# Optimization experiments

Measured on AMD Instinct MI355X. Metric: run time of the kernel, lower is better.

The kernel has to match this reference:

```python
import jax, jax.numpy as jnp
import numpy as np

B, S, D, H = 4, 1024, 512, 16
HD = D // H
SCALE = 1.0 / np.sqrt(HD).astype(np.float32)


def setup_inputs() -> dict:
    key = jax.random.key(0)
    ks = jax.random.split(key, 20)
    std = 1.0 / np.sqrt(D).astype(np.float32)
    def W(k):
        return jax.random.normal(k, (D, D), jnp.float32) * std
    def b(k):
        return jax.random.normal(k, (D,), jnp.float32) * 0.01
    return {
        "x": jax.random.normal(ks[0], (B, S, D), jnp.float32),
        "ln_g": jnp.ones((D,), jnp.float32),
        "ln_b": jnp.zeros((D,), jnp.float32),
        "Wfa": W(ks[1]), "bfa": b(ks[2]),
        "Whp": W(ks[3]), "bhp": b(ks[4]),
        "Wmg": W(ks[5]), "bmg": b(ks[6]),
        "Wq": W(ks[7]), "bq": b(ks[8]),
        "Wk": W(ks[9]), "bk": b(ks[10]),
        "Wv": W(ks[11]), "bv": b(ks[12]),
        "Wo": W(ks[13]), "bo": b(ks[14]),
    }


def reference(x, ln_g, ln_b, Wfa, bfa, Whp, bhp, Wmg, bmg, Wq, bq, Wk, bk, Wv, bv, Wo, bo):
    residual = x
    # LayerNorm
    mu = jnp.mean(x, axis=-1, keepdims=True)
    var = jnp.mean(jnp.square(x - mu), axis=-1, keepdims=True)
    xn = (x - mu) * jax.lax.rsqrt(var + 1e-5) * ln_g + ln_b

    def lin(h, W, bb):
        return h @ W + bb

    fa = lin(xn, Wfa, bfa).reshape(B, S, H, HD)            # flow anchors, per-head
    hf = lin(xn, Whp, bhp).reshape(B, S, H, HD)            # hierarchical features
    mg = jax.nn.sigmoid(lin(xn, Wmg, bmg)).reshape(B, S, H, HD)  # memory gates
    q = lin(xn, Wq, bq).reshape(B, S, H, HD)
    k = lin(xn, Wk, bk).reshape(B, S, H, HD)
    v = lin(xn, Wv, bv).reshape(B, S, H, HD)

    # anchor weights: softmax over the SEQUENCE axis (dim=1)
    anchor_w = jax.nn.softmax(fa, axis=1)                  # [B,S,H,HD]
    k_weighted = k * anchor_w

    scores = jnp.einsum("bshd,bthd->bsht", q, k_weighted) * SCALE  # [B,S,H,T]
    probs = jax.nn.softmax(scores, axis=2)                 # softmax over HEAD axis (non-standard)
    attn = jnp.einsum("bsht,bthd->bshd", probs, v)         # [B,S,H,HD]

    out = (attn * mg + hf).reshape(B, S, D)
    out = lin(out, Wo, bo)
    return out + residual
```

## Files before the change

### kernel.cpp

```cpp
#include <hip/hip_runtime.h>
#include <hip/hip_bf16.h>
#include <math.h>

#define BB 4
#define SS 1024
#define DD 512
#define HH 16
#define HD 32
#define NTOK (BB * SS)
#define NELEM ((size_t)NTOK * DD)
#define SCALE 0.17677669529663687f
#define SCLOG2E 0.25505526082484745f

typedef __attribute__((ext_vector_type(8))) __bf16 bf16x8;
typedef __attribute__((ext_vector_type(4))) __bf16 bf16x4;
typedef __attribute__((ext_vector_type(4))) float f32x4;
typedef __attribute__((ext_vector_type(4))) unsigned short us4;
typedef __attribute__((ext_vector_type(4))) short s16x4;

__device__ __forceinline__ void gload16(const void* g, void* l) {
    __builtin_amdgcn_global_load_lds(
        (const __attribute__((address_space(1))) void*)g,
        (__attribute__((address_space(3))) void*)l, 16, 0, 0);
}

__global__ __launch_bounds__(256) void ln_kernel(const float* __restrict__ x,
                                                 const float* __restrict__ g,
                                                 const float* __restrict__ bta,
                                                 __bf16* __restrict__ xn) {
    int row = blockIdx.x;
    int tid = threadIdx.x;
    const float* xr = x + (size_t)row * DD;
    float2 v = *reinterpret_cast<const float2*>(&xr[tid * 2]);
    float s1 = v.x + v.y;
    float s2 = v.x * v.x + v.y * v.y;
    for (int off = 32; off > 0; off >>= 1) {
        s1 += __shfl_down(s1, off);
        s2 += __shfl_down(s2, off);
    }
    __shared__ float r1[4], r2[4];
    int w = tid >> 6;
    if ((tid & 63) == 0) { r1[w] = s1; r2[w] = s2; }
    __syncthreads();
    s1 = r1[0] + r1[1] + r1[2] + r1[3];
    s2 = r2[0] + r2[1] + r2[2] + r2[3];
    float mu = s1 * (1.0f / DD);
    float var = s2 * (1.0f / DD) - mu * mu;
    float rstd = rsqrtf(var + 1e-5f);
    float2 gg = *reinterpret_cast<const float2*>(&g[tid * 2]);
    float2 bb = *reinterpret_cast<const float2*>(&bta[tid * 2]);
    __bf16* xp = xn + (size_t)row * DD + tid * 2;
    xp[0] = (__bf16)((v.x - mu) * rstd * gg.x + bb.x);
    xp[1] = (__bf16)((v.y - mu) * rstd * gg.y + bb.y);
}

struct W7 { const float* p[7]; };

__global__ __launch_bounds__(256) void wprep(W7 wp, __bf16* __restrict__ Wt) {
    int z = blockIdx.z;
    int kt = blockIdx.x, nt = blockIdx.y;
    const float* W = wp.p[z];
    __shared__ float lds[32][33];
    int tid = threadIdx.x;
    int r = tid >> 3, c4 = (tid & 7) * 4;
    float4 vv = *reinterpret_cast<const float4*>(W + (size_t)(kt * 32 + r) * DD + nt * 32 + c4);
    lds[r][c4 + 0] = vv.x; lds[r][c4 + 1] = vv.y;
    lds[r][c4 + 2] = vv.z; lds[r][c4 + 3] = vv.w;
    __syncthreads();
    __bf16* o = Wt + (size_t)z * DD * DD + (size_t)(nt * 32 + r) * DD + kt * 32 + c4;
    o[0] = (__bf16)lds[c4 + 0][r];
    o[1] = (__bf16)lds[c4 + 1][r];
    o[2] = (__bf16)lds[c4 + 2][r];
    o[3] = (__bf16)lds[c4 + 3][r];
}

struct GemmCfg { const float* bias[6]; void* out[6]; int mode[6]; };

__global__ __launch_bounds__(256) void mfma_gemm(const __bf16* __restrict__ A,
                                                 const __bf16* __restrict__ Wt0,
                                                 GemmCfg cfg,
                                                 const float* __restrict__ resid) {
    __shared__ __align__(16) char smem[49152];
    int z = blockIdx.z;
    const char* Ab8 = (const char*)A;
    const char* Bb8 = (const char*)(Wt0 + (size_t)z * DD * DD);
    int tid = threadIdx.x;
    int l = tid & 63, wid = tid >> 6;
    int lr = l & 15, lg = l >> 4;
    int wm = wid >> 1, wn = wid & 1;
    int bm = blockIdx.x * 128;
    int bn = blockIdx.y * 64;

    f32x4 acc[4][2];
#pragma unroll
    for (int i = 0; i < 4; ++i)
#pragma unroll
        for (int j = 0; j < 2; ++j) acc[i][j] = (f32x4){0.f, 0.f, 0.f, 0.f};

    auto stage = [&](int k0, int bsel) {
        char* base = smem + bsel * 24576;
#pragma unroll
        for (int i = 0; i < 4; ++i) {
            int r = wid * 32 + i * 8 + (l >> 3);
            int cb = ((l & 7) * 16) ^ ((r & 7) << 4);
            gload16(Ab8 + (size_t)(bm + r) * 1024 + k0 * 2 + cb,
                    base + wid * 4096 + i * 1024);
        }
#pragma unroll
        for (int i = 0; i < 2; ++i) {
            int r = wid * 16 + i * 8 + (l >> 3);
            int cb = ((l & 7) * 16) ^ ((r & 7) << 4);
            gload16(Bb8 + (size_t)(bn + r) * 1024 + k0 * 2 + cb,
                    base + 16384 + wid * 2048 + i * 1024);
        }
    };

    stage(0, 0);
    for (int ks = 0; ks < 8; ++ks) {
        __builtin_amdgcn_s_barrier();
        if (ks < 7) {
            stage((ks + 1) * 64, (ks + 1) & 1);
            asm volatile("s_waitcnt vmcnt(6)" ::: "memory");
        } else {
            asm volatile("s_waitcnt vmcnt(0)" ::: "memory");
        }
        __builtin_amdgcn_s_barrier();
        __builtin_amdgcn_sched_barrier(0);

        const char* cbase = smem + (ks & 1) * 24576;
#pragma unroll
        for (int kk = 0; kk < 2; ++kk) {
            bf16x8 af[4], wf[2];
#pragma unroll
            for (int mi = 0; mi < 4; ++mi) {
                int m = wm * 64 + mi * 16 + lr;
                af[mi] = *reinterpret_cast<const bf16x8*>(
                    cbase + m * 128 + ((kk * 64 + lg * 16) ^ ((m & 7) << 4)));
            }
#pragma unroll
            for (int ni = 0; ni < 2; ++ni) {
                int n = wn * 32 + ni * 16 + lr;
                wf[ni] = *reinterpret_cast<const bf16x8*>(
                    cbase + 16384 + n * 128 + ((kk * 64 + lg * 16) ^ ((n & 7) << 4)));
            }
            __builtin_amdgcn_s_setprio(1);
#pragma unroll
            for (int mi = 0; mi < 4; ++mi)
#pragma unroll
                for (int ni = 0; ni < 2; ++ni)
                    acc[mi][ni] = __builtin_amdgcn_mfma_f32_16x16x32_bf16(af[mi], wf[ni], acc[mi][ni], 0, 0, 0);
            __builtin_amdgcn_s_setprio(0);
        }
    }

    int bmw = bm + wm * 64;
    int bnw = bn + wn * 32;
    int mode = cfg.mode[z];
    const float* bias = cfg.bias[z];
    float bv[2] = {bias[bnw + lr], bias[bnw + 16 + lr]};
#pragma unroll
    for (int mi = 0; mi < 4; ++mi) {
#pragma unroll
        for (int ni = 0; ni < 2; ++ni) {
#pragma unroll
            for (int r = 0; r < 4; ++r) {
                int row = bmw + mi * 16 + lg * 4 + r;
                int col = bnw + ni * 16 + lr;
                float val = acc[mi][ni][r] + bv[ni];
                if (mode == 0) {
                    if (resid) val += resid[(size_t)row * DD + col];
                    ((float*)cfg.out[z])[(size_t)row * DD + col] = val;
                } else if (mode == 1) {
                    val = 1.0f / (1.0f + expf(-val));
                    ((__bf16*)cfg.out[z])[(size_t)row * DD + col] = (__bf16)val;
                } else if (mode == 3) {
                    ((__bf16*)cfg.out[z])[(size_t)row * DD + col] = (__bf16)(val * SCLOG2E);
                } else {
                    ((__bf16*)cfg.out[z])[(size_t)row * DD + col] = (__bf16)val;
                }
            }
        }
    }
}

__global__ __launch_bounds__(256) void anchor_partial(const __bf16* __restrict__ fa,
                                                      float* __restrict__ pmax,
                                                      float* __restrict__ psum) {
    int tx = threadIdx.x;
    int ty = threadIdx.y;
    int c = blockIdx.x * 64 + tx;
    int b = blockIdx.y;
    int sc = blockIdx.z;
    const __bf16* base = fa + ((size_t)(b * SS + sc * 256)) * DD + c;
    float m = -1e30f;
    for (int i = ty; i < 256; i += 4) m = fmaxf(m, (float)base[(size_t)i * DD]);
    __shared__ float red[4][64];
    red[ty][tx] = m;
    __syncthreads();
    float cm = fmaxf(fmaxf(red[0][tx], red[1][tx]), fmaxf(red[2][tx], red[3][tx]));
    float s = 0.f;
    for (int i = ty; i < 256; i += 4) s += expf((float)base[(size_t)i * DD] - cm);
    __syncthreads();
    red[ty][tx] = s;
    __syncthreads();
    if (ty == 0) {
        float tot = red[0][tx] + red[1][tx] + red[2][tx] + red[3][tx];
        int o = (b * 4 + sc) * DD + c;
        pmax[o] = cm;
        psum[o] = tot;
    }
}

__global__ __launch_bounds__(256) void anchor_merge(const float* __restrict__ pmax,
                                                    const float* __restrict__ psum,
                                                    float2* __restrict__ smscale) {
    int idx = blockIdx.x * 256 + threadIdx.x;
    int b = idx >> 9;
    int c = idx & 511;
    float M = -1e30f;
#pragma unroll
    for (int j = 0; j < 4; ++j) M = fmaxf(M, pmax[(b * 4 + j) * DD + c]);
    float Z = 0.f;
#pragma unroll
    for (int j = 0; j < 4; ++j) Z += psum[(b * 4 + j) * DD + c] * expf(pmax[(b * 4 + j) * DD + c] - M);
    smscale[idx] = make_float2(M, 1.0f / Z);
}

__global__ __launch_bounds__(256) void kweight(const __bf16* __restrict__ fa,
                                               const __bf16* __restrict__ kin,
                                               const float2* __restrict__ sm,
                                               __bf16* __restrict__ kw) {
    size_t f = ((size_t)blockIdx.x * 256 + threadIdx.x) * 8;
    int b = (int)(f >> 19);
    int c = (int)(f & 511);
    bf16x8 fv = *reinterpret_cast<const bf16x8*>(fa + f);
    bf16x8 kv = *reinterpret_cast<const bf16x8*>(kin + f);
    const float2* smb = sm + b * DD + c;
    bf16x8 o;
#pragma unroll
    for (int j = 0; j < 8; ++j) {
        float2 s = smb[j];
        o[j] = (__bf16)((float)kv[j] * expf((float)fv[j] - s.x) * s.y);
    }
    *reinterpret_cast<bf16x8*>(kw + f) = o;
}

__global__ __launch_bounds__(256) void vtrans(const __bf16* __restrict__ v,
                                              __bf16* __restrict__ vt) {
    int t0 = blockIdx.x * 32;
    int h = blockIdx.y;
    int b = blockIdx.z;
    __shared__ unsigned short lds[32][33];
    int tid = threadIdx.x;
    int r = tid >> 3, c4 = (tid & 7) * 4;
    const unsigned short* vp = (const unsigned short*)v + ((size_t)(b * SS + t0 + r)) * DD + h * 32 + c4;
    us4 val = *reinterpret_cast<const us4*>(vp);
    lds[r][c4 + 0] = val[0]; lds[r][c4 + 1] = val[1];
    lds[r][c4 + 2] = val[2]; lds[r][c4 + 3] = val[3];
    __syncthreads();
    us4 o;
    o[0] = lds[c4 + 0][r]; o[1] = lds[c4 + 1][r];
    o[2] = lds[c4 + 2][r]; o[3] = lds[c4 + 3][r];
    unsigned short* op = (unsigned short*)vt +
        ((size_t)(b * 128 + ((t0 + c4) >> 3)) * 512 + h * 32 + r) * 8 + (c4 & 7);
    *reinterpret_cast<us4*>(op) = o;
}

struct P4 { __bf16* p[4]; };

__global__ __launch_bounds__(512) void attn_mfma(const __bf16* __restrict__ q,
                                                 const __bf16* __restrict__ kw,
                                                 const __bf16* __restrict__ vt,
                                                 P4 ps) {
    __shared__ __align__(16) char smem[65536];
    int sgq = blockIdx.x;
    int b = blockIdx.y;
    int tp = blockIdx.z;
    int tid = threadIdx.x;
    int wid = tid >> 6;
    int lane = tid & 63;
    int lg = lane >> 4;
    int lr = lane & 15;
    int sgrp = wid & 1;
    int hq = wid >> 1;
    int hbase = hq * 4;
    int s0 = (sgq * 2 + sgrp) * 16;

    const __bf16* qbase = q + ((size_t)(b * SS + s0 + lr)) * DD + lg * 8;
    const char* kwb8 = (const char*)kw + (size_t)b * SS * DD * 2;
    const char* vtb8 = (const char*)vt + (size_t)b * 128 * 8192;

    bf16x8 qf[4];
#pragma unroll
    for (int hi = 0; hi < 4; ++hi)
        qf[hi] = *reinterpret_cast<const bf16x8*>(qbase + (hbase + hi) * 32);

    f32x4 acc[4][2];
#pragma unroll
    for (int hi = 0; hi < 4; ++hi) {
        acc[hi][0] = (f32x4){0.f, 0.f, 0.f, 0.f};
        acc[hi][1] = (f32x4){0.f, 0.f, 0.f, 0.f};
    }

    auto stage = [&](int tbase, int bsel) {
#pragma unroll
        for (int i = 0; i < 2; ++i) {
            int row = wid + i * 8;
            int colb = (lane * 16) ^ ((row & 15) << 4);
            gload16(kwb8 + (size_t)(tbase + row) * 1024 + colb,
                    smem + bsel * 16384 + row * 1024);
        }
#pragma unroll
        for (int i = 0; i < 2; ++i) {
            int blkid = wid + i * 8;
            gload16(vtb8 + (size_t)((tbase >> 3) + (blkid >> 3)) * 8192 + (blkid & 7) * 1024 + lane * 16,
                    smem + 32768 + bsel * 16384 + blkid * 1024);
        }
    };

    int tbase0 = tp * 256;
    stage(tbase0, 0);

    for (int tc = 0; tc < 256; tc += 16) {
        int cur = (tc >> 4) & 1;
        char* kwbuf = smem + cur * 16384;
        char* vtbuf = smem + 32768 + cur * 16384;
        char* xch = kwbuf + sgrp * 4096;

        asm volatile("s_waitcnt vmcnt(2)" ::: "memory");
        __builtin_amdgcn_s_barrier();
        __builtin_amdgcn_sched_barrier(0);

        f32x4 sc[4];
        bf16x8 ka[4];
#pragma unroll
        for (int hi = 0; hi < 4; ++hi)
            ka[hi] = *reinterpret_cast<const bf16x8*>(
                kwbuf + lr * 1024 + ((((hbase + hi) * 64) + lg * 16) ^ (lr << 4)));
        __builtin_amdgcn_s_setprio(1);
#pragma unroll
        for (int hi = 0; hi < 4; ++hi) {
            f32x4 z = (f32x4){0.f, 0.f, 0.f, 0.f};
            sc[hi] = __builtin_amdgcn_mfma_f32_16x16x32_bf16(ka[hi], qf[hi], z, 0, 0, 0);
        }
        __builtin_amdgcn_s_setprio(0);

        __builtin_amdgcn_s_barrier();
        __builtin_amdgcn_sched_barrier(0);

#pragma unroll
        for (int hi = 0; hi < 4; ++hi)
#pragma unroll
            for (int r = 0; r < 4; ++r) sc[hi][r] = exp2f(sc[hi][r]);
        f32x4 zsp = sc[0] + sc[1] + sc[2] + sc[3];
        *reinterpret_cast<f32x4*>(xch + hq * 1024 + lane * 16) = zsp;
        if (tc + 16 < 256) stage(tbase0 + tc + 16, cur ^ 1);
        asm volatile("s_waitcnt lgkmcnt(0)" ::: "memory");
        __builtin_amdgcn_s_barrier();
        __builtin_amdgcn_sched_barrier(0);

        f32x4 zt = zsp;
#pragma unroll
        for (int p = 0; p < 4; ++p)
            if (p != hq) zt += *reinterpret_cast<const f32x4*>(xch + p * 1024 + lane * 16);
        float inv[4];
#pragma unroll
        for (int r = 0; r < 4; ++r) inv[r] = __builtin_amdgcn_rcpf(zt[r]);
        bf16x4 pA[4];
#pragma unroll
        for (int hi = 0; hi < 4; ++hi)
#pragma unroll
            for (int r = 0; r < 4; ++r) pA[hi][r] = (__bf16)(sc[hi][r] * inv[r]);

        if (tc + 16 < 256) {
            asm volatile("s_waitcnt vmcnt(4)" ::: "memory");
        } else {
            asm volatile("s_waitcnt vmcnt(0)" ::: "memory");
        }
        __builtin_amdgcn_s_barrier();
        __builtin_amdgcn_sched_barrier(0);

        const char* vb = vtbuf + (lg >> 1) * 8192 + (lg & 1) * 8;
#pragma unroll
        for (int hi = 0; hi < 4; hi += 2) {
            s16x4 vf[4];
#pragma unroll
            for (int j = 0; j < 2; ++j) {
                int h = hbase + hi + j;
                vf[2 * j + 0] = *reinterpret_cast<const s16x4*>(vb + (h * 32 + lr) * 16);
                vf[2 * j + 1] = *reinterpret_cast<const s16x4*>(vb + (h * 32 + 16 + lr) * 16);
            }
            __builtin_amdgcn_s_setprio(1);
#pragma unroll
            for (int j = 0; j < 2; ++j) {
                s16x4 pa = __builtin_bit_cast(s16x4, pA[hi + j]);
                acc[hi + j][0] = __builtin_amdgcn_mfma_f32_16x16x16bf16_1k(pa, vf[2 * j + 0], acc[hi + j][0], 0, 0, 0);
                acc[hi + j][1] = __builtin_amdgcn_mfma_f32_16x16x16bf16_1k(pa, vf[2 * j + 1], acc[hi + j][1], 0, 0, 0);
            }
            __builtin_amdgcn_s_setprio(0);
        }
    }

    __bf16* pb = ps.p[tp] + ((size_t)(b * SS + s0)) * DD;
#pragma unroll
    for (int hi = 0; hi < 4; ++hi)
#pragma unroll
        for (int dh = 0; dh < 2; ++dh)
#pragma unroll
            for (int r = 0; r < 4; ++r)
                pb[(size_t)(lg * 4 + r) * DD + (hbase + hi) * 32 + dh * 16 + lr] = (__bf16)acc[hi][dh][r];
}

struct P4c { const __bf16* p[4]; };

__global__ __launch_bounds__(256) void combine_kernel(P4c ps,
                                                      const __bf16* __restrict__ mg,
                                                      const __bf16* __restrict__ hf,
                                                      __bf16* __restrict__ comb) {
    size_t f = ((size_t)blockIdx.x * 256 + threadIdx.x) * 8;
    float accv[8] = {0.f, 0.f, 0.f, 0.f, 0.f, 0.f, 0.f, 0.f};
#pragma unroll
    for (int i = 0; i < 4; ++i) {
        bf16x8 v = *reinterpret_cast<const bf16x8*>(ps.p[i] + f);
#pragma unroll
        for (int j = 0; j < 8; ++j) accv[j] += (float)v[j];
    }
    bf16x8 m = *reinterpret_cast<const bf16x8*>(mg + f);
    bf16x8 hh = *reinterpret_cast<const bf16x8*>(hf + f);
    bf16x8 o;
#pragma unroll
    for (int j = 0; j < 8; ++j) o[j] = (__bf16)(accv[j] * (float)m[j] + (float)hh[j]);
    *reinterpret_cast<bf16x8*>(comb + f) = o;
}

extern "C" void kernel_launch(void* const* d_in, const int* in_sizes, int n_in,
                              void* d_out, int out_size, void* d_ws, size_t ws_size,
                              hipStream_t stream) {
    const float* x    = (const float*)d_in[0];
    const float* ln_g = (const float*)d_in[1];
    const float* ln_b = (const float*)d_in[2];
    const float* Wfa  = (const float*)d_in[3];  const float* bfa = (const float*)d_in[4];
    const float* Whp  = (const float*)d_in[5];  const float* bhp = (const float*)d_in[6];
    const float* Wmg  = (const float*)d_in[7];  const float* bmg = (const float*)d_in[8];
    const float* Wq   = (const float*)d_in[9];  const float* bq  = (const float*)d_in[10];
    const float* Wk   = (const float*)d_in[11]; const float* bk  = (const float*)d_in[12];
    const float* Wv   = (const float*)d_in[13]; const float* bv  = (const float*)d_in[14];
    const float* Wo   = (const float*)d_in[15]; const float* bo  = (const float*)d_in[16];
    float* out = (float*)d_out;

    char* w8 = (char*)d_ws;
    __bf16* Wt   = (__bf16*)(w8 + ((size_t) 0 << 20));
    __bf16* xn   = (__bf16*)(w8 + ((size_t) 4 << 20));
    __bf16* fa   = (__bf16*)(w8 + ((size_t) 8 << 20));
    __bf16* hf   = (__bf16*)(w8 + ((size_t)12 << 20));
    __bf16* mg   = (__bf16*)(w8 + ((size_t)16 << 20));
    __bf16* q    = (__bf16*)(w8 + ((size_t)20 << 20));
    __bf16* k    = (__bf16*)(w8 + ((size_t)24 << 20));
    __bf16* v    = (__bf16*)(w8 + ((size_t)28 << 20));
    __bf16* kw   = (__bf16*)(w8 + ((size_t)32 << 20));
    __bf16* vt   = (__bf16*)(w8 + ((size_t)36 << 20));
    P4 ps;
    ps.p[0] = (__bf16*)(w8 + ((size_t) 4 << 20));
    ps.p[1] = (__bf16*)(w8 + ((size_t) 8 << 20));
    ps.p[2] = (__bf16*)(w8 + ((size_t)24 << 20));
    ps.p[3] = (__bf16*)(w8 + ((size_t)28 << 20));
    __bf16* comb = (__bf16*)(w8 + ((size_t)56 << 20));
    float* pmax  = (float*) (w8 + ((size_t)60 << 20));
    float* psum  = pmax + 16 * DD;
    float2* smsc = (float2*)(psum + 16 * DD);

    ln_kernel<<<NTOK, 256, 0, stream>>>(x, ln_g, ln_b, xn);

    W7 wp; wp.p[0]=Wfa; wp.p[1]=Whp; wp.p[2]=Wmg; wp.p[3]=Wq; wp.p[4]=Wk; wp.p[5]=Wv; wp.p[6]=Wo;
    wprep<<<dim3(16, 16, 7), 256, 0, stream>>>(wp, Wt);

    GemmCfg cfg;
    cfg.bias[0]=bfa; cfg.out[0]=fa; cfg.mode[0]=2;
    cfg.bias[1]=bhp; cfg.out[1]=hf; cfg.mode[1]=2;
    cfg.bias[2]=bmg; cfg.out[2]=mg; cfg.mode[2]=1;
    cfg.bias[3]=bq;  cfg.out[3]=q;  cfg.mode[3]=3;
    cfg.bias[4]=bk;  cfg.out[4]=k;  cfg.mode[4]=2;
    cfg.bias[5]=bv;  cfg.out[5]=v;  cfg.mode[5]=2;
    mfma_gemm<<<dim3(32, 8, 6), 256, 0, stream>>>(xn, Wt, cfg, nullptr);

    anchor_partial<<<dim3(8, 4, 4), dim3(64, 4), 0, stream>>>(fa, pmax, psum);
    anchor_merge<<<8, 256, 0, stream>>>(pmax, psum, smsc);
    kweight<<<1024, 256, 0, stream>>>(fa, k, smsc, kw);

    vtrans<<<dim3(32, 16, 4), 256, 0, stream>>>(v, vt);

    attn_mfma<<<dim3(32, 4, 4), 512, 0, stream>>>(q, kw, vt, ps);

    P4c pc;
    for (int i = 0; i < 4; ++i) pc.p[i] = ps.p[i];
    combine_kernel<<<1024, 256, 0, stream>>>(pc, mg, hf, comb);

    GemmCfg cfg2;
    for (int i = 0; i < 6; ++i) { cfg2.bias[i]=bo; cfg2.out[i]=out; cfg2.mode[i]=0; }
    mfma_gemm<<<dim3(32, 8, 1), 256, 0, stream>>>(comb, Wt + (size_t)6 * DD * DD, cfg2, x);
}
```

Baseline: 132.9 us.

## Share A tile across three projection weights in a fused QKV-style GEMM

Result: faster. 122.4 us (median of 2 runs) (-8.0%).

```diff
diff --git a/kernel.cpp b/kernel.cpp
--- a/kernel.cpp
+++ b/kernel.cpp
@@ -76,6 +76,124 @@
 
 struct GemmCfg { const float* bias[6]; void* out[6]; int mode[6]; };
 
+__global__ __launch_bounds__(256) void mfma_gemm3(const __bf16* __restrict__ A,
+                                                  const __bf16* __restrict__ Wt0,
+                                                  GemmCfg cfg) {
+    __shared__ __align__(16) char smem[81920];
+    int zh = blockIdx.z;
+    const char* Ab8 = (const char*)A;
+    int tid = threadIdx.x;
+    int l = tid & 63, wid = tid >> 6;
+    int lr = l & 15, lg = l >> 4;
+    int wm = wid >> 1, wn = wid & 1;
+    int bm = blockIdx.x * 128;
+    int bn = blockIdx.y * 64;
+    const char* Bb8[3];
+#pragma unroll
+    for (int z = 0; z < 3; ++z)
+        Bb8[z] = (const char*)(Wt0 + (size_t)(zh * 3 + z) * DD * DD);
+
+    f32x4 acc[3][4][2];
+#pragma unroll
+    for (int z = 0; z < 3; ++z)
+#pragma unroll
+        for (int i = 0; i < 4; ++i)
+#pragma unroll
+            for (int j = 0; j < 2; ++j) acc[z][i][j] = (f32x4){0.f, 0.f, 0.f, 0.f};
+
+    auto stage = [&](int k0, int bsel) {
+        char* base = smem + bsel * 40960;
+#pragma unroll
+        for (int i = 0; i < 4; ++i) {
+            int r = wid * 32 + i * 8 + (l >> 3);
+            int cb = ((l & 7) * 16) ^ ((r & 7) << 4);
+            gload16(Ab8 + (size_t)(bm + r) * 1024 + k0 * 2 + cb,
+                    base + wid * 4096 + i * 1024);
+        }
+#pragma unroll
+        for (int z = 0; z < 3; ++z)
+#pragma unroll
+            for (int i = 0; i < 2; ++i) {
+                int r = wid * 16 + i * 8 + (l >> 3);
+                int cb = ((l & 7) * 16) ^ ((r & 7) << 4);
+                gload16(Bb8[z] + (size_t)(bn + r) * 1024 + k0 * 2 + cb,
+                        base + 16384 + z * 8192 + wid * 2048 + i * 1024);
+            }
+    };
+
+    stage(0, 0);
+    for (int ks = 0; ks < 8; ++ks) {
+        __builtin_amdgcn_s_barrier();
+        if (ks < 7) {
+            stage((ks + 1) * 64, (ks + 1) & 1);
+            asm volatile("s_waitcnt vmcnt(10)" ::: "memory");
+        } else {
+            asm volatile("s_waitcnt vmcnt(0)" ::: "memory");
+        }
+        __builtin_amdgcn_s_barrier();
+        __builtin_amdgcn_sched_barrier(0);
+
+        const char* cbase = smem + (ks & 1) * 40960;
+#pragma unroll
+        for (int kk = 0; kk < 2; ++kk) {
+            bf16x8 af[4];
+#pragma unroll
+            for (int mi = 0; mi < 4; ++mi) {
+                int m = wm * 64 + mi * 16 + lr;
+                af[mi] = *reinterpret_cast<const bf16x8*>(
+                    cbase + m * 128 + ((kk * 64 + lg * 16) ^ ((m & 7) << 4)));
+            }
+#pragma unroll
+            for (int z = 0; z < 3; ++z) {
+                bf16x8 wf[2];
+#pragma unroll
+                for (int ni = 0; ni < 2; ++ni) {
+                    int n = wn * 32 + ni * 16 + lr;
+                    wf[ni] = *reinterpret_cast<const bf16x8*>(
+                        cbase + 16384 + z * 8192 + n * 128 + ((kk * 64 + lg * 16) ^ ((n & 7) << 4)));
+                }
+                __builtin_amdgcn_s_setprio(1);
+#pragma unroll
+                for (int mi = 0; mi < 4; ++mi)
+#pragma unroll
+                    for (int ni = 0; ni < 2; ++ni)
+                        acc[z][mi][ni] = __builtin_amdgcn_mfma_f32_16x16x32_bf16(af[mi], wf[ni], acc[z][mi][ni], 0, 0, 0);
+                __builtin_amdgcn_s_setprio(0);
+            }
+        }
+    }
+
+    int bmw = bm + wm * 64;
+    int bnw = bn + wn * 32;
+#pragma unroll
+    for (int z = 0; z < 3; ++z) {
+        int slot = zh * 3 + z;
+        int mode = cfg.mode[slot];
+        const float* bias = cfg.bias[slot];
+        float bv[2] = {bias[bnw + lr], bias[bnw + 16 + lr]};
+#pragma unroll
+        for (int mi = 0; mi < 4; ++mi) {
+#pragma unroll
+            for (int ni = 0; ni < 2; ++ni) {
+#pragma unroll
+                for (int r = 0; r < 4; ++r) {
+                    int row = bmw + mi * 16 + lg * 4 + r;
+                    int col = bnw + ni * 16 + lr;
+                    float val = acc[z][mi][ni][r] + bv[ni];
+                    if (mode == 1) {
+                        val = 1.0f / (1.0f + expf(-val));
+                        ((__bf16*)cfg.out[slot])[(size_t)row * DD + col] = (__bf16)val;
+                    } else if (mode == 3) {
+                        ((__bf16*)cfg.out[slot])[(size_t)row * DD + col] = (__bf16)(val * SCLOG2E);
+                    } else {
+                        ((__bf16*)cfg.out[slot])[(size_t)row * DD + col] = (__bf16)val;
+                    }
+                }
+            }
+        }
+    }
+}
+
 __global__ __launch_bounds__(256) void mfma_gemm(const __bf16* __restrict__ A,
                                                  const __bf16* __restrict__ Wt0,
                                                  GemmCfg cfg,
@@ -170,11 +288,6 @@
                 if (mode == 0) {
                     if (resid) val += resid[(size_t)row * DD + col];
                     ((float*)cfg.out[z])[(size_t)row * DD + col] = val;
-                } else if (mode == 1) {
-                    val = 1.0f / (1.0f + expf(-val));
-                    ((__bf16*)cfg.out[z])[(size_t)row * DD + col] = (__bf16)val;
-                } else if (mode == 3) {
-                    ((__bf16*)cfg.out[z])[(size_t)row * DD + col] = (__bf16)(val * SCLOG2E);
                 } else {
                     ((__bf16*)cfg.out[z])[(size_t)row * DD + col] = (__bf16)val;
                 }
@@ -481,7 +594,7 @@
     cfg.bias[3]=bq;  cfg.out[3]=q;  cfg.mode[3]=3;
     cfg.bias[4]=bk;  cfg.out[4]=k;  cfg.mode[4]=2;
     cfg.bias[5]=bv;  cfg.out[5]=v;  cfg.mode[5]=2;
-    mfma_gemm<<<dim3(32, 8, 6), 256, 0, stream>>>(xn, Wt, cfg, nullptr);
+    mfma_gemm3<<<dim3(32, 8, 2), 256, 0, stream>>>(xn, Wt, cfg);
 
     anchor_partial<<<dim3(8, 4, 4), dim3(64, 4), 0, stream>>>(fa, pmax, psum);
     anchor_merge<<<8, 256, 0, stream>>>(pmax, psum, smsc);
```
